# Performance work log

Measured on AMD Instinct MI355X. Metric: run time of the kernel, lower is better.

## Reference

```python
import jax, jax.numpy as jnp
import numpy as np

B, S, D, DK, DV = 8, 2048, 256, 128, 128

def setup_inputs() -> dict:
    key = jax.random.key(0)
    ks = jax.random.split(key, 9)
    return {
        "x_q": jax.random.normal(ks[0], (B, S, D), jnp.float32),
        "x_k": jax.random.normal(ks[1], (B, S, D), jnp.float32),
        "x_v": jax.random.normal(ks[2], (B, S, D), jnp.float32),
        "Wq": jax.random.normal(ks[3], (D, DK), jnp.float32) * (1.0 / np.sqrt(D)),
        "bq": jax.random.normal(ks[4], (DK,), jnp.float32) * 0.02,
        "Wk": jax.random.normal(ks[5], (D, DK), jnp.float32) * (1.0 / np.sqrt(D)),
        "bk": jax.random.normal(ks[6], (DK,), jnp.float32) * 0.02,
        "Wv": jax.random.normal(ks[7], (D, DV), jnp.float32) * (1.0 / np.sqrt(D)),
        "bv": jax.random.normal(ks[8], (DV,), jnp.float32) * 0.02,
    }

def reference(x_q, x_k, x_v, Wq, bq, Wk, bk, Wv, bv):
    # Dense projections: [B,S,D] @ [D,dk] + bias
    q = jnp.einsum("bsd,dk->bsk", x_q, Wq) + bq
    k = jnp.einsum("bsd,dk->bsk", x_k, Wk) + bk
    v = jnp.einsum("bsd,dv->bsv", x_v, Wv) + bv
    scale = 1.0 / np.sqrt(Wq.shape[1]).astype(np.float32)  # 1/sqrt(d_k)
    scores = jnp.einsum("bqk,bsk->bqs", q, k) * scale       # [B,S,S]
    attn = jax.nn.softmax(scores, axis=-1)
    return jnp.einsum("bqs,bsv->bqv", attn, v)               # [B,S,d_v]
```

## Files before the change

### kernel.cpp

```cpp
#include <hip/hip_runtime.h>
#include <stdint.h>

typedef float    f32x4  __attribute__((ext_vector_type(4)));
typedef float    f32x16 __attribute__((ext_vector_type(16)));
typedef _Float16 f16x8  __attribute__((ext_vector_type(8)));
typedef _Float16 f16x4  __attribute__((ext_vector_type(4)));
typedef unsigned int u32x4 __attribute__((ext_vector_type(4)));

#define SPLIT 4
#define NTILES 16

__device__ __forceinline__ f32x4 mfma16(f16x8 a, f16x8 b, f32x4 c) {
    return __builtin_amdgcn_mfma_f32_16x16x32_f16(a, b, c, 0, 0, 0);
}
__device__ __forceinline__ f32x16 mfma32(f16x8 a, f16x8 b, f32x16 c) {
    return __builtin_amdgcn_mfma_f32_32x32x16_f16(a, b, c, 0, 0, 0);
}
__device__ __forceinline__ void gll16(const _Float16* g, _Float16* l) {
    __builtin_amdgcn_global_load_lds(
        (const __attribute__((address_space(1))) void*)g,
        (__attribute__((address_space(3))) void*)l, 16, 0, 0);
}

__global__ __launch_bounds__(256) void prep_weights(
    const float* __restrict__ Wq, const float* __restrict__ Wk,
    const float* __restrict__ Wv, _Float16* __restrict__ wt) {
    __shared__ float Ls[64 * 65];
    const int bx = blockIdx.x;
    const int w  = bx >> 3, t = bx & 7;
    const int k0 = (t >> 1) * 64, n0 = (t & 1) * 64;
    const float* W = (w == 0) ? Wq : (w == 1) ? Wk : Wv;
    const int tid = threadIdx.x;
    #pragma unroll
    for (int i = 0; i < 16; i++) {
        int idx = i * 256 + tid;
        int r = idx >> 6, c = idx & 63;
        Ls[r * 65 + c] = W[(k0 + r) * 128 + n0 + c];
    }
    __syncthreads();
    #pragma unroll
    for (int i = 0; i < 16; i++) {
        int idx = i * 256 + tid;
        int r2 = idx >> 6, c2 = idx & 63;
        wt[w * 32768 + (n0 + r2) * 256 + k0 + c2] = (_Float16)Ls[c2 * 65 + r2];
    }
}

__global__ __launch_bounds__(256) void proj_kernel(
    const float* __restrict__ xq, const float* __restrict__ xk,
    const float* __restrict__ xv, const _Float16* __restrict__ wt,
    const float* __restrict__ bq, const float* __restrict__ bk,
    const float* __restrict__ bv,
    _Float16* __restrict__ qo, _Float16* __restrict__ ko,
    _Float16* __restrict__ vt)
{
    const int mode = blockIdx.y;
    const float*    X    = mode == 0 ? xq : mode == 1 ? xk : xv;
    const float*    bias = mode == 0 ? bq : mode == 1 ? bk : bv;
    const _Float16* W    = wt + mode * 32768;

    __shared__ __align__(16) _Float16 Ls[128 * 66];

    const int tid  = threadIdx.x;
    const int wave = tid >> 6, lane = tid & 63;
    const int ln   = lane & 15, qd = lane >> 4;
    const int row0 = blockIdx.x * 64 + wave * 16;

    const float*    xrow = X + (size_t)(row0 + ln) * 256 + qd * 8;
    const _Float16* wb   = W + ln * 256 + qd * 8;

    f32x4 acc[8];
    #pragma unroll
    for (int i = 0; i < 8; i++) acc[i] = (f32x4){0.f, 0.f, 0.f, 0.f};

    #pragma unroll
    for (int kk = 0; kk < 8; kk++) {
        f32x4 a0 = *(const f32x4*)(xrow + kk * 32);
        f32x4 a1 = *(const f32x4*)(xrow + kk * 32 + 4);
        f16x8 af;
        af[0] = (_Float16)a0[0]; af[1] = (_Float16)a0[1];
        af[2] = (_Float16)a0[2]; af[3] = (_Float16)a0[3];
        af[4] = (_Float16)a1[0]; af[5] = (_Float16)a1[1];
        af[6] = (_Float16)a1[2]; af[7] = (_Float16)a1[3];
        #pragma unroll
        for (int nt = 0; nt < 8; nt++) {
            f16x8 bf = *(const f16x8*)(wb + nt * 4096 + kk * 32);
            acc[nt] = mfma16(af, bf, acc[nt]);
        }
    }

    const float SC = 0.08838834764831845f * 1.4426950408889634f;
    if (mode != 2) {
        _Float16* Y = mode == 0 ? qo : ko;
        #pragma unroll
        for (int nt = 0; nt < 8; nt++) {
            int col = nt * 16 + ln;
            float bb = bias[col];
            #pragma unroll
            for (int r = 0; r < 4; r++) {
                int orow = row0 + qd * 4 + r;
                float val = acc[nt][r] + bb;
                if (mode == 0) val *= SC;
                Y[(size_t)orow * 128 + col] = (_Float16)val;
            }
        }
    } else {
        #pragma unroll
        for (int nt = 0; nt < 8; nt++) {
            int col = nt * 16 + ln;
            float bb = bias[col];
            #pragma unroll
            for (int r = 0; r < 4; r++) {
                int srow = wave * 16 + qd * 4 + r;
                Ls[col * 66 + srow] = (_Float16)(acc[nt][r] + bb);
            }
        }
        __syncthreads();
        const int bb2 = row0 >> 11;
        const int s0  = (blockIdx.x * 64) & 2047;
        #pragma unroll
        for (int i = 0; i < 4; i++) {
            int g  = i * 256 + tid;
            int dv = g >> 3, off = (g & 7) * 8;
            f16x8 v8 = *(const f16x8*)&Ls[dv * 66 + off];
            *(f16x8*)(vt + ((size_t)(bb2 * 128 + dv)) * 2048 + s0 + off) = v8;
        }
    }
}

__global__ __launch_bounds__(256, 3) void attn_kernel(
    const _Float16* __restrict__ qp, const _Float16* __restrict__ kp,
    const _Float16* __restrict__ vtp, _Float16* __restrict__ opart,
    float2* __restrict__ ml)
{
    const int bid = blockIdx.x;
    const int gx  = bid & 7;
    const int q0i = (bid >> 3) & 15;
    const int gg  = bid >> 7;
    const int g   = gg * 8 + gx;
    const int b   = g >> 2;
    const int z   = g & 3;
    const int q0  = q0i * 128;

    const int tid  = threadIdx.x;
    const int wave = tid >> 6, lane = tid & 63;
    const int ln   = lane & 31, h = lane >> 5;

    __shared__ __align__(16) _Float16 smem[16896];

    int koff[8], voff[2][4];
    #pragma unroll
    for (int kb = 0; kb < 8; kb++)
        koff[kb] = ln * 128 + (((kb * 2 + h) ^ (ln & 15)) * 8);
    #pragma unroll
    for (int kb2 = 0; kb2 < 2; kb2++)
        #pragma unroll
        for (int dvb = 0; dvb < 4; dvb++)
            voff[kb2][dvb] = 8192 + (dvb * 32 + ln) * 32 + (kb2 * 2 + h) * 8;
    int kidx[2], vidx[2], dst[2];
    #pragma unroll
    for (int j = 0; j < 2; j++) {
        int p = wave * 128 + j * 64 + lane;
        int r = p >> 4, c = p & 15;
        kidx[j] = r * 128 + ((c ^ (r & 15)) * 8);
        vidx[j] = (p >> 2) * 2048 + (p & 3) * 8;
        dst[j]  = (wave * 128 + j * 64) * 8;
    }

    const _Float16* qbase =
        qp + (size_t)(b * 2048 + q0 + wave * 32 + ln) * 128 + h * 8;
    f16x8 qf[8];
    #pragma unroll
    for (int kb = 0; kb < 8; kb++) qf[kb] = *(const f16x8*)(qbase + kb * 16);

    f32x16 o[4];
    #pragma unroll
    for (int i = 0; i < 4; i++) o[i] = (f32x16){};
    float m_run = -1e30f, l_run = 0.f;

    const _Float16* kbase = kp + (size_t)b * 2048 * 128;
    const _Float16* vbase = vtp + (size_t)b * 128 * 2048;
    const int kt0 = z * NTILES;

    auto stage = [&](int kt, int buf) {
        const _Float16* ks = kbase + (size_t)kt * 4096;
        const _Float16* vs = vbase + kt * 32;
        _Float16* kdst = smem + buf * 4096;
        _Float16* vdst = smem + 8192 + buf * 4096;
        #pragma unroll
        for (int j = 0; j < 2; j++) {
            gll16(ks + kidx[j], kdst + dst[j]);
            gll16(vs + vidx[j], vdst + dst[j]);
        }
    };

    auto do_tile = [&](const int BUF) {
        const int KO = BUF * 4096, VO = BUF * 4096;
        f32x16 sc = (f32x16){};
        #pragma unroll
        for (int kb = 0; kb < 8; kb++) {
            f16x8 kf = *(const f16x8*)&smem[KO + koff[kb]];
            sc = mfma32(kf, qf[kb], sc);
        }
        float t = sc[0];
        #pragma unroll
        for (int i = 1; i < 16; i++) t = fmaxf(t, sc[i]);
        t = fmaxf(t, __shfl_xor(t, 32));
        const float mnew  = fmaxf(m_run, t);
        const float alpha = exp2f(m_run - mnew);

        f16x4 phg[4];
        float ssum = 0.f;
        #pragma unroll
        for (int gi = 0; gi < 4; gi++) {
            #pragma unroll
            for (int e = 0; e < 4; e++) {
                float p = exp2f(sc[gi * 4 + e] - mnew);
                ssum += p;
                phg[gi][e] = (_Float16)p;
            }
        }
        ssum += __shfl_xor(ssum, 32);
        l_run = l_run * alpha + ssum;
        m_run = mnew;

        if (__any(alpha < 1.0f)) {
            #pragma unroll
            for (int dvb = 0; dvb < 4; dvb++) o[dvb] *= alpha;
        }

        #pragma unroll
        for (int kb2 = 0; kb2 < 2; kb2++) {
            f16x4 own0 = phg[2 * kb2], own1 = phg[2 * kb2 + 1];
            f16x4 send = h ? own0 : own1;
            unsigned long long sv = __builtin_bit_cast(unsigned long long, send);
            unsigned long long rv = __shfl_xor(sv, 32);
            f16x4 recv = __builtin_bit_cast(f16x4, rv);
            f16x4 lo = h ? recv : own0;
            f16x4 hi = h ? own1 : recv;
            f16x8 bf = __builtin_shufflevector(lo, hi, 0, 1, 2, 3, 4, 5, 6, 7);
            #pragma unroll
            for (int dvb = 0; dvb < 4; dvb++) {
                f16x8 vf = *(const f16x8*)&smem[VO + voff[kb2][dvb]];
                o[dvb] = mfma32(vf, bf, o[dvb]);
            }
        }
    };

    stage(kt0, 0);
    #pragma unroll 1
    for (int ht = 0; ht < NTILES / 2; ht++) {
        __syncthreads();
        if (2 * ht + 1 < NTILES) stage(kt0 + 2 * ht + 1, 1);
        do_tile(0);
        __syncthreads();
        if (2 * ht + 2 < NTILES) stage(kt0 + 2 * ht + 2, 0);
        do_tile(1);
    }

    __syncthreads();
    _Float16* pw = smem + wave * 4224;
    #pragma unroll
    for (int dvb = 0; dvb < 4; dvb++) {
        #pragma unroll
        for (int gi = 0; gi < 4; gi++) {
            f16x4 w4;
            #pragma unroll
            for (int e = 0; e < 4; e++) w4[e] = (_Float16)o[dvb][gi * 4 + e];
            *(f16x4*)&pw[ln * 132 + dvb * 32 + gi * 8 + h * 4] = w4;
        }
    }
    const size_t prow = (size_t)(z * 8 + b) * 2048 + q0 + wave * 32;
    __builtin_amdgcn_s_waitcnt(0);
    #pragma unroll
    for (int p = 0; p < 2; p++) {
        int q = p * 16 + (lane >> 2), part = lane & 3;
        #pragma unroll
        for (int i2 = 0; i2 < 4; i2++) {
            f16x8 v8 = *(const f16x8*)&pw[q * 132 + part * 8 + i2 * 32];
            *(f16x8*)(opart + (prow + q) * 128 + part * 8 + i2 * 32) = v8;
        }
    }
    if (lane < 32) {
        float2 v; v.x = m_run; v.y = l_run;
        ml[prow + ln] = v;
    }
}

__global__ __launch_bounds__(256) void merge_kernel(
    const _Float16* __restrict__ opart, const float2* __restrict__ ml,
    float* __restrict__ out)
{
    const int t = threadIdx.x;
    const int r = t >> 4, cg = t & 15;
    const size_t row = (size_t)blockIdx.x * 16 + r;

    float M = -1e30f;
    #pragma unroll
    for (int zi = 0; zi < SPLIT; zi++)
        M = fmaxf(M, ml[(size_t)zi * 16384 + row].x);
    float L = 0.f;
    float acc[8] = {0.f, 0.f, 0.f, 0.f, 0.f, 0.f, 0.f, 0.f};
    #pragma unroll
    for (int zi = 0; zi < SPLIT; zi++) {
        float2 p = ml[(size_t)zi * 16384 + row];
        float w = exp2f(p.x - M);
        L += w * p.y;
        f16x8 v = *(const f16x8*)&opart[((size_t)zi * 16384 + row) * 128 + cg * 8];
        #pragma unroll
        for (int j = 0; j < 8; j++) acc[j] += w * (float)v[j];
    }
    const float inv = 1.0f / L;
    float* op = out + row * 128 + cg * 8;
    f32x4 lo = (f32x4){acc[0] * inv, acc[1] * inv, acc[2] * inv, acc[3] * inv};
    f32x4 hi = (f32x4){acc[4] * inv, acc[5] * inv, acc[6] * inv, acc[7] * inv};
    *(f32x4*)op = lo;
    *(f32x4*)(op + 4) = hi;
}

extern "C" void kernel_launch(void* const* d_in, const int* in_sizes, int n_in,
                              void* d_out, int out_size, void* d_ws, size_t ws_size,
                              hipStream_t stream) {
    const float* xq = (const float*)d_in[0];
    const float* xk = (const float*)d_in[1];
    const float* xv = (const float*)d_in[2];
    const float* Wq = (const float*)d_in[3];
    const float* bq = (const float*)d_in[4];
    const float* Wk = (const float*)d_in[5];
    const float* bk = (const float*)d_in[6];
    const float* Wv = (const float*)d_in[7];
    const float* bv = (const float*)d_in[8];
    float* out = (float*)d_out;

    char* ws = (char*)d_ws;
    _Float16* wt    = (_Float16*)ws;
    _Float16* qo    = (_Float16*)(ws + 196608);
    _Float16* ko    = (_Float16*)(ws + 196608 + 4194304);
    _Float16* vt    = (_Float16*)(ws + 196608 + 2 * 4194304);
    float2*   ml    = (float2*)  (ws + 196608 + 3 * 4194304);
    _Float16* opart = (_Float16*)(ws + 196608 + 3 * 4194304 + 1048576);

    hipLaunchKernelGGL(prep_weights, dim3(24), dim3(256), 0, stream,
                       Wq, Wk, Wv, wt);
    hipLaunchKernelGGL(proj_kernel, dim3(256, 3), dim3(256), 0, stream,
                       xq, xk, xv, wt, bq, bk, bv, qo, ko, vt);
    hipLaunchKernelGGL(attn_kernel, dim3(16 * 8 * SPLIT), dim3(256), 0, stream,
                       qo, ko, vt, opart, ml);
    hipLaunchKernelGGL(merge_kernel, dim3(1024), dim3(256), 0, stream,
                       opart, ml, out);
}
```

Baseline: 163.2 us.

## Load K and V fragments directly from global memory instead of LDS staging

Replaces the double-buffered global_load_lds staging of K and V tiles, along with its block-wide barriers, with per-wave direct global loads into registers. The next K tile is prefetched into registers during softmax, and V fragments are read straight from global memory. This removes the LDS traffic and __syncthreads, but each of the four waves now fetches the same K/V data separately through the cache, and the V loads sit on the critical path with no prefetch.

```diff
diff --git a/kernel.cpp b/kernel.cpp
--- a/kernel.cpp
+++ b/kernel.cpp
@@ -15,11 +15,6 @@
 }
 __device__ __forceinline__ f32x16 mfma32(f16x8 a, f16x8 b, f32x16 c) {
     return __builtin_amdgcn_mfma_f32_32x32x16_f16(a, b, c, 0, 0, 0);
-}
-__device__ __forceinline__ void gll16(const _Float16* g, _Float16* l) {
-    __builtin_amdgcn_global_load_lds(
-        (const __attribute__((address_space(1))) void*)g,
-        (__attribute__((address_space(3))) void*)l, 16, 0, 0);
 }
 
 __global__ __launch_bounds__(256) void prep_weights(
@@ -148,25 +143,6 @@
 
     __shared__ __align__(16) _Float16 smem[16896];
 
-    int koff[8], voff[2][4];
-    #pragma unroll
-    for (int kb = 0; kb < 8; kb++)
-        koff[kb] = ln * 128 + (((kb * 2 + h) ^ (ln & 15)) * 8);
-    #pragma unroll
-    for (int kb2 = 0; kb2 < 2; kb2++)
-        #pragma unroll
-        for (int dvb = 0; dvb < 4; dvb++)
-            voff[kb2][dvb] = 8192 + (dvb * 32 + ln) * 32 + (kb2 * 2 + h) * 8;
-    int kidx[2], vidx[2], dst[2];
-    #pragma unroll
-    for (int j = 0; j < 2; j++) {
-        int p = wave * 128 + j * 64 + lane;
-        int r = p >> 4, c = p & 15;
-        kidx[j] = r * 128 + ((c ^ (r & 15)) * 8);
-        vidx[j] = (p >> 2) * 2048 + (p & 3) * 8;
-        dst[j]  = (wave * 128 + j * 64) * 8;
-    }
-
     const _Float16* qbase =
         qp + (size_t)(b * 2048 + q0 + wave * 32 + ln) * 128 + h * 8;
     f16x8 qf[8];
@@ -178,35 +154,34 @@
     for (int i = 0; i < 4; i++) o[i] = (f32x16){};
     float m_run = -1e30f, l_run = 0.f;
 
-    const _Float16* kbase = kp + (size_t)b * 2048 * 128;
-    const _Float16* vbase = vtp + (size_t)b * 128 * 2048;
     const int kt0 = z * NTILES;
-
-    auto stage = [&](int kt, int buf) {
-        const _Float16* ks = kbase + (size_t)kt * 4096;
-        const _Float16* vs = vbase + kt * 32;
-        _Float16* kdst = smem + buf * 4096;
-        _Float16* vdst = smem + 8192 + buf * 4096;
-        #pragma unroll
-        for (int j = 0; j < 2; j++) {
-            gll16(ks + kidx[j], kdst + dst[j]);
-            gll16(vs + vidx[j], vdst + dst[j]);
-        }
-    };
-
-    auto do_tile = [&](const int BUF) {
-        const int KO = BUF * 4096, VO = BUF * 4096;
+    const _Float16* kptr =
+        kp + ((size_t)b * 2048 + (size_t)kt0 * 32 + ln) * 128 + h * 8;
+    const _Float16* vptr =
+        vtp + ((size_t)b * 128 + ln) * 2048 + (size_t)kt0 * 32 + h * 8;
+
+    f16x8 kf[8];
+    #pragma unroll
+    for (int kb = 0; kb < 8; kb++) kf[kb] = *(const f16x8*)(kptr + kb * 16);
+
+    #pragma unroll 1
+    for (int t = 0; t < NTILES; t++) {
         f32x16 sc = (f32x16){};
         #pragma unroll
-        for (int kb = 0; kb < 8; kb++) {
-            f16x8 kf = *(const f16x8*)&smem[KO + koff[kb]];
-            sc = mfma32(kf, qf[kb], sc);
-        }
-        float t = sc[0];
-        #pragma unroll
-        for (int i = 1; i < 16; i++) t = fmaxf(t, sc[i]);
-        t = fmaxf(t, __shfl_xor(t, 32));
-        const float mnew  = fmaxf(m_run, t);
+        for (int kb = 0; kb < 8; kb++) sc = mfma32(kf[kb], qf[kb], sc);
+
+        if (t + 1 < NTILES) {
+            const _Float16* np = kptr + (size_t)(t + 1) * 4096;
+            #pragma unroll
+            for (int kb = 0; kb < 8; kb++)
+                kf[kb] = *(const f16x8*)(np + kb * 16);
+        }
+
+        float tmax = sc[0];
+        #pragma unroll
+        for (int i = 1; i < 16; i++) tmax = fmaxf(tmax, sc[i]);
+        tmax = fmaxf(tmax, __shfl_xor(tmax, 32));
+        const float mnew  = fmaxf(m_run, tmax);
         const float alpha = exp2f(m_run - mnew);
 
         f16x4 phg[4];
@@ -229,6 +204,7 @@
             for (int dvb = 0; dvb < 4; dvb++) o[dvb] *= alpha;
         }
 
+        const _Float16* vtile = vptr + t * 32;
         #pragma unroll
         for (int kb2 = 0; kb2 < 2; kb2++) {
             f16x4 own0 = phg[2 * kb2], own1 = phg[2 * kb2 + 1];
@@ -241,24 +217,12 @@
             f16x8 bf = __builtin_shufflevector(lo, hi, 0, 1, 2, 3, 4, 5, 6, 7);
             #pragma unroll
             for (int dvb = 0; dvb < 4; dvb++) {
-                f16x8 vf = *(const f16x8*)&smem[VO + voff[kb2][dvb]];
+                f16x8 vf = *(const f16x8*)(vtile + (size_t)dvb * 65536 + kb2 * 16);
                 o[dvb] = mfma32(vf, bf, o[dvb]);
             }
         }
-    };
-
-    stage(kt0, 0);
-    #pragma unroll 1
-    for (int ht = 0; ht < NTILES / 2; ht++) {
-        __syncthreads();
-        if (2 * ht + 1 < NTILES) stage(kt0 + 2 * ht + 1, 1);
-        do_tile(0);
-        __syncthreads();
-        if (2 * ht + 2 < NTILES) stage(kt0 + 2 * ht + 2, 0);
-        do_tile(1);
-    }
-
-    __syncthreads();
+    }
+
     _Float16* pw = smem + wave * 4224;
     #pragma unroll
     for (int dvb = 0; dvb < 4; dvb++) {
```

Result: slower. 196.4 us (+20.3%).

## Deepen K/V prefetch to four LDS buffers, swizzle V, prioritize MFMA

Applied to the files above, without the earlier changes.

Replaces the double-buffered K/V staging with a four-slot ring so two tiles are in flight. Each phase waits with an explicit vmcnt and a bare s_barrier instead of __syncthreads, which is meant to hide global-to-LDS latency better. It also XOR-swizzles the V tile layout in LDS to cut bank conflicts on the PV reads, and raises wave priority around the MFMA blocks. The cost is that LDS per block roughly doubles to 64KB, which can lower the number of resident blocks per CU below the launch-bounds target of 3.

```diff
diff --git a/kernel.cpp b/kernel.cpp
--- a/kernel.cpp
+++ b/kernel.cpp
@@ -5,7 +5,6 @@
 typedef float    f32x16 __attribute__((ext_vector_type(16)));
 typedef _Float16 f16x8  __attribute__((ext_vector_type(8)));
 typedef _Float16 f16x4  __attribute__((ext_vector_type(4)));
-typedef unsigned int u32x4 __attribute__((ext_vector_type(4)));
 
 #define SPLIT 4
 #define NTILES 16
@@ -146,24 +145,25 @@
     const int wave = tid >> 6, lane = tid & 63;
     const int ln   = lane & 31, h = lane >> 5;
 
-    __shared__ __align__(16) _Float16 smem[16896];
+    __shared__ __align__(16) _Float16 smem[32768];
 
     int koff[8], voff[2][4];
     #pragma unroll
     for (int kb = 0; kb < 8; kb++)
         koff[kb] = ln * 128 + (((kb * 2 + h) ^ (ln & 15)) * 8);
+    const int vsw = (ln >> 1) & 3;
     #pragma unroll
     for (int kb2 = 0; kb2 < 2; kb2++)
         #pragma unroll
         for (int dvb = 0; dvb < 4; dvb++)
-            voff[kb2][dvb] = 8192 + (dvb * 32 + ln) * 32 + (kb2 * 2 + h) * 8;
+            voff[kb2][dvb] = (dvb * 32 + ln) * 32 + (((kb2 * 2 + h) ^ vsw) * 8);
     int kidx[2], vidx[2], dst[2];
     #pragma unroll
     for (int j = 0; j < 2; j++) {
         int p = wave * 128 + j * 64 + lane;
         int r = p >> 4, c = p & 15;
         kidx[j] = r * 128 + ((c ^ (r & 15)) * 8);
-        vidx[j] = (p >> 2) * 2048 + (p & 3) * 8;
+        vidx[j] = (p >> 2) * 2048 + (((p & 3) ^ ((p >> 3) & 3)) * 8);
         dst[j]  = (wave * 128 + j * 64) * 8;
     }
 
@@ -186,7 +186,7 @@
         const _Float16* ks = kbase + (size_t)kt * 4096;
         const _Float16* vs = vbase + kt * 32;
         _Float16* kdst = smem + buf * 4096;
-        _Float16* vdst = smem + 8192 + buf * 4096;
+        _Float16* vdst = smem + 16384 + buf * 4096;
         #pragma unroll
         for (int j = 0; j < 2; j++) {
             gll16(ks + kidx[j], kdst + dst[j]);
@@ -195,13 +195,15 @@
     };
 
     auto do_tile = [&](const int BUF) {
-        const int KO = BUF * 4096, VO = BUF * 4096;
+        const int KO = BUF * 4096, VO = 16384 + BUF * 4096;
         f32x16 sc = (f32x16){};
+        __builtin_amdgcn_s_setprio(1);
         #pragma unroll
         for (int kb = 0; kb < 8; kb++) {
             f16x8 kf = *(const f16x8*)&smem[KO + koff[kb]];
             sc = mfma32(kf, qf[kb], sc);
         }
+        __builtin_amdgcn_s_setprio(0);
         float t = sc[0];
         #pragma unroll
         for (int i = 1; i < 16; i++) t = fmaxf(t, sc[i]);
@@ -239,24 +241,42 @@
             f16x4 lo = h ? recv : own0;
             f16x4 hi = h ? own1 : recv;
             f16x8 bf = __builtin_shufflevector(lo, hi, 0, 1, 2, 3, 4, 5, 6, 7);
+            __builtin_amdgcn_s_setprio(1);
             #pragma unroll
             for (int dvb = 0; dvb < 4; dvb++) {
                 f16x8 vf = *(const f16x8*)&smem[VO + voff[kb2][dvb]];
                 o[dvb] = mfma32(vf, bf, o[dvb]);
             }
+            __builtin_amdgcn_s_setprio(0);
         }
     };
 
+#define PHASE(VM, STAGE_T, STAGE_BUF, TILE_BUF)                         \
+    do {                                                                \
+        asm volatile("s_waitcnt vmcnt(" #VM ")" ::: "memory");          \
+        __builtin_amdgcn_sched_barrier(0);                              \
+        __builtin_amdgcn_s_barrier();                                   \
+        __builtin_amdgcn_sched_barrier(0);                              \
+        if ((STAGE_T) >= 0) stage(kt0 + (STAGE_T), STAGE_BUF);          \
+        do_tile(TILE_BUF);                                              \
+    } while (0)
+
     stage(kt0, 0);
+    stage(kt0 + 1, 1);
     #pragma unroll 1
-    for (int ht = 0; ht < NTILES / 2; ht++) {
-        __syncthreads();
-        if (2 * ht + 1 < NTILES) stage(kt0 + 2 * ht + 1, 1);
-        do_tile(0);
-        __syncthreads();
-        if (2 * ht + 2 < NTILES) stage(kt0 + 2 * ht + 2, 0);
-        do_tile(1);
-    }
+    for (int ht = 0; ht < 4; ht++) {
+        const int t0 = ht * 4;
+        const bool last = (ht == 3);
+        PHASE(4, t0 + 2, 2, 0);
+        PHASE(4, t0 + 3, 3, 1);
+        PHASE(4, last ? -1 : t0 + 4, 0, 2);
+        if (!last) {
+            PHASE(4, t0 + 5, 1, 3);
+        } else {
+            PHASE(0, -1, 1, 3);
+        }
+    }
+#undef PHASE
 
     __syncthreads();
     _Float16* pw = smem + wave * 4224;
```

Result: slower. 180.0 us (+10.3%).
